# Performance work log

Measured on AMD Instinct MI355X. Metric: run time of the kernel, lower is better.

The kernel has to match this reference:

```python
import jax, jax.numpy as jnp
import numpy as np

B, T, D, HEADS = 2, 2048, 1024, 16


def setup_inputs() -> dict:
    key = jax.random.key(0)
    k1, k2, k3 = jax.random.split(key, 3)
    X = jax.random.normal(k1, (B, T, D), dtype=jnp.float32)
    W_KQV = jax.random.normal(k2, (D, 3 * D), dtype=jnp.float32) * 0.02
    W_out = jax.random.normal(k3, (D, D), dtype=jnp.float32) * 0.02
    # causal additive mask: -1e9 above the diagonal, 0 elsewhere
    mask = jnp.triu(jnp.full((T, T), -1e9, dtype=jnp.float32), k=1)
    return {"X": X, "W_KQV": W_KQV, "W_out": W_out, "mask": mask, "heads": HEADS}


def reference(X, W_KQV, W_out, mask, heads):
    b, t, d = X.shape
    hd = d // heads
    res = jnp.einsum('btd,de->bte', X, W_KQV)  # [B,T,3d]
    # needle module stacks split columns in K, Q, V order
    K, Q, V = jnp.split(res, 3, axis=-1)

    def to_heads(A):  # [B,T,d] -> [B,H,T,hd]
        return A.reshape(b, t, heads, hd).transpose(0, 2, 1, 3)

    K, Q, V = to_heads(K), to_heads(Q), to_heads(V)
    # NOTE: original computes K @ Q^T (not Q @ K^T) -- reproduced faithfully
    scores = jnp.einsum('bhkd,bhqd->bhkq', K, Q) / (hd ** 0.5) + mask  # [B,H,T,T]
    attn = jax.nn.softmax(scores, axis=-1)
    ctx = jnp.einsum('bhtq,bhqd->bhtd', attn, V)  # [B,H,T,hd]
    ctx = ctx.transpose(0, 2, 1, 3).reshape(b, t, d)
    out = jnp.einsum('btd,de->bte', ctx, W_out)  # [B,T,d]
    return out, attn
```

## Files before the change

### kernel.cpp

```cpp
#include <hip/hip_runtime.h>
#include <cstddef>

constexpr int B_ = 2, T_ = 2048, D_ = 1024, H_ = 16;

typedef __attribute__((ext_vector_type(8))) short short8;
typedef __attribute__((ext_vector_type(4))) float floatx4;

__device__ inline unsigned short f2bf(float f) {
    union { float f; unsigned int u; } v; v.f = f;
    unsigned int r = v.u + 0x7fffu + ((v.u >> 16) & 1u);
    return (unsigned short)(r >> 16);
}

#define GLD_LDS16(gptr, ldsptr)                                                        \
    __builtin_amdgcn_global_load_lds(                                                  \
        (const __attribute__((address_space(1))) void*)(gptr),                         \
        (__attribute__((address_space(3))) void*)(ldsptr), 16, 0, 0)

__global__ __launch_bounds__(256) void cast_bf16(const float* __restrict__ in,
                                                 unsigned short* __restrict__ out) {
    int idx = (blockIdx.x * 256 + threadIdx.x) * 8;
    float4 a = *(const float4*)(in + idx);
    float4 b = *(const float4*)(in + idx + 4);
    unsigned short tmp[8] = {f2bf(a.x), f2bf(a.y), f2bf(a.z), f2bf(a.w),
                             f2bf(b.x), f2bf(b.y), f2bf(b.z), f2bf(b.w)};
    *(uint4*)(out + idx) = *(const uint4*)tmp;
}

__global__ __launch_bounds__(256) void transpose_cast(const float* __restrict__ W,
                                                      unsigned short* __restrict__ Wt,
                                                      int K, int N) {
    const int k0 = blockIdx.y * 64, n0 = blockIdx.x * 64;
    __shared__ float t[64][65];
    const int tid = threadIdx.x;
    const int row = tid >> 4, c4 = (tid & 15) * 4;
#pragma unroll
    for (int r = 0; r < 4; r++) {
        float4 v = *(const float4*)&W[(size_t)(k0 + row + r * 16) * N + n0 + c4];
        t[row + r * 16][c4 + 0] = v.x; t[row + r * 16][c4 + 1] = v.y;
        t[row + r * 16][c4 + 2] = v.z; t[row + r * 16][c4 + 3] = v.w;
    }
    __syncthreads();
    const int n = tid >> 2, ks = (tid & 3) * 16;
    unsigned short o[16];
#pragma unroll
    for (int i = 0; i < 16; i++) o[i] = f2bf(t[ks + i][n]);
    unsigned short* dst = Wt + (size_t)(n0 + n) * K + k0 + ks;
    *(uint4*)dst = ((const uint4*)o)[0];
    *(uint4*)(dst + 8) = ((const uint4*)o)[1];
}

template <typename CT>
__global__ __launch_bounds__(256) void gemm_bt(const unsigned short* __restrict__ A,
                                               const unsigned short* __restrict__ Bt,
                                               CT* __restrict__ C, int M, int N, int K) {
    __shared__ unsigned short As[128 * 32];
    __shared__ unsigned short Bs[128 * 32];
    const int tid = threadIdx.x;
    const int lane = tid & 63, wave = tid >> 6;
    const int quad = lane >> 4, l16 = lane & 15;
    const int wr = wave >> 1, wc = wave & 1;
    const size_t bm = (size_t)blockIdx.y * 128, bn = (size_t)blockIdx.x * 128;
    const int r0 = tid >> 2, kc0 = (tid & 3) * 8;
    const unsigned short* Ap = A + bm * K;
    const unsigned short* Bp = Bt + bn * K;
    floatx4 acc[4][4] = {};
    for (int k0 = 0; k0 < K; k0 += 32) {
        GLD_LDS16(Ap + (size_t)r0 * K + k0 + kc0, &As[tid * 8]);
        GLD_LDS16(Ap + (size_t)(r0 + 64) * K + k0 + kc0, &As[(tid + 256) * 8]);
        GLD_LDS16(Bp + (size_t)r0 * K + k0 + kc0, &Bs[tid * 8]);
        GLD_LDS16(Bp + (size_t)(r0 + 64) * K + k0 + kc0, &Bs[(tid + 256) * 8]);
        __syncthreads();
        short8 af[4], bf[4];
#pragma unroll
        for (int i = 0; i < 4; i++)
            af[i] = *(const short8*)&As[(wr * 64 + i * 16 + l16) * 32 + quad * 8];
#pragma unroll
        for (int j = 0; j < 4; j++)
            bf[j] = *(const short8*)&Bs[(wc * 64 + j * 16 + l16) * 32 + quad * 8];
#pragma unroll
        for (int i = 0; i < 4; i++)
#pragma unroll
            for (int j = 0; j < 4; j++)
                acc[i][j] = __builtin_amdgcn_mfma_f32_16x16x32_bf16(af[i], bf[j], acc[i][j], 0, 0, 0);
        __syncthreads();
    }
#pragma unroll
    for (int i = 0; i < 4; i++) {
        size_t row0 = bm + wr * 64 + i * 16 + quad * 4;
#pragma unroll
        for (int j = 0; j < 4; j++) {
            size_t col = bn + wc * 64 + j * 16 + l16;
#pragma unroll
            for (int r = 0; r < 4; r++) {
                if constexpr (sizeof(CT) == 2)
                    C[(row0 + r) * N + col] = (CT)f2bf(acc[i][j][r]);
                else
                    C[(row0 + r) * N + col] = acc[i][j][r];
            }
        }
    }
}

__global__ __launch_bounds__(256) void scores_mfma(const unsigned short* __restrict__ resb,
                                                   float* __restrict__ attn) {
    const int bh = blockIdx.z, b = bh >> 4, h = bh & 15;
    const int bk = blockIdx.y * 128, bq = blockIdx.x * 128;
    float* S = attn + (size_t)bh * T_ * T_;
    const int tid = threadIdx.x;
    if (bq > bk) {
        const float4 z = make_float4(0.f, 0.f, 0.f, 0.f);
#pragma unroll
        for (int i = 0; i < 16; i++) {
            int idx = tid + i * 256;
            int row = idx >> 5, c4 = (idx & 31) * 4;
            *(float4*)&S[(size_t)(bk + row) * T_ + bq + c4] = z;
        }
        return;
    }
    __shared__ unsigned short Ks[128 * 64];
    __shared__ unsigned short Qs[128 * 64];
    const unsigned short* Kg = resb + (size_t)b * T_ * (3 * D_) + h * 64;
    const unsigned short* Qg = Kg + D_;
    const int row = tid >> 3, dc = (tid & 7) * 8;
#pragma unroll
    for (int r = 0; r < 4; r++) {
        GLD_LDS16(Kg + (size_t)(bk + row + r * 32) * (3 * D_) + dc, &Ks[(tid + r * 256) * 8]);
        GLD_LDS16(Qg + (size_t)(bq + row + r * 32) * (3 * D_) + dc, &Qs[(tid + r * 256) * 8]);
    }
    __syncthreads();
    const int lane = tid & 63, wave = tid >> 6;
    const int quad = lane >> 4, l16 = lane & 15;
    const int wr = wave >> 1, wc = wave & 1;
    floatx4 acc[4][4] = {};
#pragma unroll
    for (int ks = 0; ks < 2; ks++) {
        short8 af[4], bf[4];
#pragma unroll
        for (int i = 0; i < 4; i++)
            af[i] = *(const short8*)&Ks[(wr * 64 + i * 16 + l16) * 64 + ks * 32 + quad * 8];
#pragma unroll
        for (int j = 0; j < 4; j++)
            bf[j] = *(const short8*)&Qs[(wc * 64 + j * 16 + l16) * 64 + ks * 32 + quad * 8];
#pragma unroll
        for (int i = 0; i < 4; i++)
#pragma unroll
            for (int j = 0; j < 4; j++)
                acc[i][j] = __builtin_amdgcn_mfma_f32_16x16x32_bf16(af[i], bf[j], acc[i][j], 0, 0, 0);
    }
#pragma unroll
    for (int i = 0; i < 4; i++) {
        int k0r = bk + wr * 64 + i * 16 + quad * 4;
#pragma unroll
        for (int j = 0; j < 4; j++) {
            int q = bq + wc * 64 + j * 16 + l16;
#pragma unroll
            for (int r = 0; r < 4; r++) {
                int k = k0r + r;
                S[(size_t)k * T_ + q] = (q > k) ? -1e9f : acc[i][j][r] * 0.125f;
            }
        }
    }
}

__global__ __launch_bounds__(256) void softmax_causal(float* __restrict__ attn) {
    const size_t row = blockIdx.x;
    const int k = (int)(row & (T_ - 1));
    const int L = ((k >> 7) + 1) << 7;
    float* p = attn + row * (size_t)T_;
    const int t = threadIdx.x;
    float v[8];
    float m = -3.0e38f;
#pragma unroll
    for (int i = 0; i < 8; i++) {
        int q = t + i * 256;
        v[i] = (q < L) ? p[q] : -1e9f;
        m = fmaxf(m, v[i]);
    }
#pragma unroll
    for (int off = 32; off > 0; off >>= 1) m = fmaxf(m, __shfl_down(m, off, 64));
    __shared__ float redm[4], reds[4];
    const int wave = t >> 6, lane = t & 63;
    if (lane == 0) redm[wave] = m;
    __syncthreads();
    m = fmaxf(fmaxf(redm[0], redm[1]), fmaxf(redm[2], redm[3]));
    float s = 0.f;
#pragma unroll
    for (int i = 0; i < 8; i++) {
        v[i] = __expf(v[i] - m);
        s += v[i];
    }
#pragma unroll
    for (int off = 32; off > 0; off >>= 1) s += __shfl_down(s, off, 64);
    if (lane == 0) reds[wave] = s;
    __syncthreads();
    s = reds[0] + reds[1] + reds[2] + reds[3];
    const float inv = 1.0f / s;
#pragma unroll
    for (int i = 0; i < 8; i++) {
        int q = t + i * 256;
        if (q < L) p[q] = v[i] * inv;
    }
}

__global__ __launch_bounds__(256) void transpose_v(const unsigned short* __restrict__ resb,
                                                   unsigned short* __restrict__ Vt) {
    const int bh = blockIdx.y, b = bh >> 4, h = bh & 15;
    const int q0 = blockIdx.x * 64;
    __shared__ unsigned short t[64][66];
    const int tid = threadIdx.x;
    const unsigned short* Vg = resb + (size_t)b * T_ * (3 * D_) + 2 * D_ + h * 64;
    const int q = tid >> 3, c8 = (tid & 7) * 8;
#pragma unroll
    for (int r = 0; r < 2; r++) {
        int qq = q + r * 32;
        short8 v = *(const short8*)(Vg + (size_t)(q0 + qq) * (3 * D_) + c8);
#pragma unroll
        for (int i = 0; i < 8; i++) t[qq][c8 + i] = (unsigned short)v[i];
    }
    __syncthreads();
    const int c = tid >> 2, qs = (tid & 3) * 16;
    unsigned short o[16];
#pragma unroll
    for (int i = 0; i < 16; i++) o[i] = t[qs + i][c];
    unsigned short* dst = Vt + ((size_t)bh * 64 + c) * T_ + q0 + qs;
    *(uint4*)dst = ((const uint4*)o)[0];
    *(uint4*)(dst + 8) = ((const uint4*)o)[1];
}

__global__ __launch_bounds__(256) void ctx_mfma(const float* __restrict__ attn,
                                                const unsigned short* __restrict__ Vt,
                                                unsigned short* __restrict__ ctxb) {
    const int bh = blockIdx.y, b = bh >> 4, h = bh & 15;
    const int bt = blockIdx.x * 128;
    const float* Ag = attn + (size_t)bh * T_ * T_;
    const unsigned short* Bg = Vt + (size_t)bh * 64 * T_;
    __shared__ unsigned short As[128 * 40];
    __shared__ unsigned short Bs[64 * 32];
    const int tid = threadIdx.x;
    const int lane = tid & 63, wave = tid >> 6;
    const int quad = lane >> 4, l16 = lane & 15;
    const int wr = wave >> 1, wc = wave & 1;
    const int arow = tid >> 1, aq = (tid & 1) * 16;
    const int brow = tid >> 2, bq8 = (tid & 3) * 8;
    floatx4 acc[4][2] = {};
    const int qend = bt + 128;
    for (int q0 = 0; q0 < qend; q0 += 32) {
        const float* src = Ag + (size_t)(bt + arow) * T_ + q0 + aq;
        float4 v0 = *(const float4*)src;
        float4 v1 = *(const float4*)(src + 4);
        float4 v2 = *(const float4*)(src + 8);
        float4 v3 = *(const float4*)(src + 12);
        unsigned short tmp[16] = {f2bf(v0.x), f2bf(v0.y), f2bf(v0.z), f2bf(v0.w),
                                  f2bf(v1.x), f2bf(v1.y), f2bf(v1.z), f2bf(v1.w),
                                  f2bf(v2.x), f2bf(v2.y), f2bf(v2.z), f2bf(v2.w),
                                  f2bf(v3.x), f2bf(v3.y), f2bf(v3.z), f2bf(v3.w)};
        *(uint4*)&As[arow * 40 + aq] = ((const uint4*)tmp)[0];
        *(uint4*)&As[arow * 40 + aq + 8] = ((const uint4*)tmp)[1];
        GLD_LDS16(Bg + (size_t)brow * T_ + q0 + bq8, &Bs[tid * 8]);
        __syncthreads();
        short8 af[4], bf[2];
#pragma unroll
        for (int i = 0; i < 4; i++)
            af[i] = *(const short8*)&As[(wr * 64 + i * 16 + l16) * 40 + quad * 8];
#pragma unroll
        for (int j = 0; j < 2; j++)
            bf[j] = *(const short8*)&Bs[(wc * 32 + j * 16 + l16) * 32 + quad * 8];
#pragma unroll
        for (int i = 0; i < 4; i++)
#pragma unroll
            for (int j = 0; j < 2; j++)
                acc[i][j] = __builtin_amdgcn_mfma_f32_16x16x32_bf16(af[i], bf[j], acc[i][j], 0, 0, 0);
        __syncthreads();
    }
#pragma unroll
    for (int i = 0; i < 4; i++) {
        size_t t0 = (size_t)bt + wr * 64 + i * 16 + quad * 4;
#pragma unroll
        for (int j = 0; j < 2; j++) {
            int c = wc * 32 + j * 16 + l16;
#pragma unroll
            for (int r = 0; r < 4; r++)
                ctxb[((size_t)b * T_ + t0 + r) * D_ + h * 64 + c] = f2bf(acc[i][j][r]);
        }
    }
}

extern "C" void kernel_launch(void* const* d_in, const int* in_sizes, int n_in,
                              void* d_out, int out_size, void* d_ws, size_t ws_size,
                              hipStream_t stream) {
    const float* X = (const float*)d_in[0];
    const float* W_KQV = (const float*)d_in[1];
    const float* W_out = (const float*)d_in[2];
    float* out = (float*)d_out;
    float* attn = (float*)d_out + (size_t)B_ * T_ * D_;

    char* ws = (char*)d_ws;
    unsigned short* Xb = (unsigned short*)ws;
    unsigned short* Wt = (unsigned short*)(ws + (8u << 20));
    unsigned short* Wot = (unsigned short*)(ws + (14u << 20));
    unsigned short* resb = (unsigned short*)(ws + (16u << 20));
    unsigned short* Vt = (unsigned short*)(ws + (40u << 20));
    unsigned short* ctxb = (unsigned short*)(ws + (48u << 20));

    cast_bf16<<<(B_ * T_ * D_) / (8 * 256), 256, 0, stream>>>(X, Xb);
    transpose_cast<<<dim3((3 * D_) / 64, D_ / 64), 256, 0, stream>>>(W_KQV, Wt, D_, 3 * D_);
    transpose_cast<<<dim3(D_ / 64, D_ / 64), 256, 0, stream>>>(W_out, Wot, D_, D_);

    gemm_bt<unsigned short><<<dim3((3 * D_) / 128, (B_ * T_) / 128), 256, 0, stream>>>(
        Xb, Wt, resb, B_ * T_, 3 * D_, D_);

    transpose_v<<<dim3(T_ / 64, B_ * H_), 256, 0, stream>>>(resb, Vt);
    scores_mfma<<<dim3(T_ / 128, T_ / 128, B_ * H_), 256, 0, stream>>>(resb, attn);
    softmax_causal<<<B_ * H_ * T_, 256, 0, stream>>>(attn);
    ctx_mfma<<<dim3(T_ / 128, B_ * H_), 256, 0, stream>>>(attn, Vt, ctxb);

    gemm_bt<float><<<dim3(D_ / 128, (B_ * T_) / 128), 256, 0, stream>>>(
        ctxb, Wot, out, B_ * T_, D_, D_);
}
```

Baseline: 874.8 us.

## Fuse scores, softmax and context into one two-pass attention kernel; swizzle GEMM LDS

Replaces the separate scores, softmax and context kernels with one fused kernel per 128-row key tile. A first pass computes running row max and sum, and a second pass recomputes the scores, writes the normalized probabilities and accumulates P·V from LDS. This removes the extra read-modify-write passes over the large fp32 attention matrix, and the re-read of it in fp32. The GEMM now uses 64-wide K steps with an XOR-swizzled LDS layout and a two-blocks-per-CU launch bound. The cost is recomputing QK^T twice, and only 512 blocks with uneven per-block work because of the causal mask.

```diff
diff --git a/kernel.cpp b/kernel.cpp
--- a/kernel.cpp
+++ b/kernel.cpp
@@ -51,38 +51,48 @@
 }
 
 template <typename CT>
-__global__ __launch_bounds__(256) void gemm_bt(const unsigned short* __restrict__ A,
-                                               const unsigned short* __restrict__ Bt,
-                                               CT* __restrict__ C, int M, int N, int K) {
-    __shared__ unsigned short As[128 * 32];
-    __shared__ unsigned short Bs[128 * 32];
+__global__ __launch_bounds__(256, 2) void gemm_bt(const unsigned short* __restrict__ A,
+                                                  const unsigned short* __restrict__ Bt,
+                                                  CT* __restrict__ C, int M, int N, int K) {
+    __shared__ unsigned short As[128 * 64];
+    __shared__ unsigned short Bs[128 * 64];
     const int tid = threadIdx.x;
     const int lane = tid & 63, wave = tid >> 6;
     const int quad = lane >> 4, l16 = lane & 15;
     const int wr = wave >> 1, wc = wave & 1;
     const size_t bm = (size_t)blockIdx.y * 128, bn = (size_t)blockIdx.x * 128;
-    const int r0 = tid >> 2, kc0 = (tid & 3) * 8;
     const unsigned short* Ap = A + bm * K;
     const unsigned short* Bp = Bt + bn * K;
+    const int srow = tid >> 3, sc = tid & 7;
     floatx4 acc[4][4] = {};
-    for (int k0 = 0; k0 < K; k0 += 32) {
-        GLD_LDS16(Ap + (size_t)r0 * K + k0 + kc0, &As[tid * 8]);
-        GLD_LDS16(Ap + (size_t)(r0 + 64) * K + k0 + kc0, &As[(tid + 256) * 8]);
-        GLD_LDS16(Bp + (size_t)r0 * K + k0 + kc0, &Bs[tid * 8]);
-        GLD_LDS16(Bp + (size_t)(r0 + 64) * K + k0 + kc0, &Bs[(tid + 256) * 8]);
-        __syncthreads();
-        short8 af[4], bf[4];
-#pragma unroll
-        for (int i = 0; i < 4; i++)
-            af[i] = *(const short8*)&As[(wr * 64 + i * 16 + l16) * 32 + quad * 8];
-#pragma unroll
-        for (int j = 0; j < 4; j++)
-            bf[j] = *(const short8*)&Bs[(wc * 64 + j * 16 + l16) * 32 + quad * 8];
-#pragma unroll
-        for (int i = 0; i < 4; i++)
-#pragma unroll
-            for (int j = 0; j < 4; j++)
-                acc[i][j] = __builtin_amdgcn_mfma_f32_16x16x32_bf16(af[i], bf[j], acc[i][j], 0, 0, 0);
+    for (int k0 = 0; k0 < K; k0 += 64) {
+#pragma unroll
+        for (int it = 0; it < 4; it++) {
+            int rr = srow + it * 32;
+            int soff = k0 + ((sc ^ (rr & 7)) << 3);
+            GLD_LDS16(Ap + (size_t)rr * K + soff, &As[(tid + it * 256) * 8]);
+            GLD_LDS16(Bp + (size_t)rr * K + soff, &Bs[(tid + it * 256) * 8]);
+        }
+        __syncthreads();
+#pragma unroll
+        for (int ks = 0; ks < 2; ks++) {
+            short8 af[4], bf[4];
+#pragma unroll
+            for (int i = 0; i < 4; i++) {
+                int row = wr * 64 + i * 16 + l16, cf = ks * 4 + quad;
+                af[i] = *(const short8*)&As[row * 64 + ((cf ^ (row & 7)) << 3)];
+            }
+#pragma unroll
+            for (int j = 0; j < 4; j++) {
+                int row = wc * 64 + j * 16 + l16, cf = ks * 4 + quad;
+                bf[j] = *(const short8*)&Bs[row * 64 + ((cf ^ (row & 7)) << 3)];
+            }
+#pragma unroll
+            for (int i = 0; i < 4; i++)
+#pragma unroll
+                for (int j = 0; j < 4; j++)
+                    acc[i][j] = __builtin_amdgcn_mfma_f32_16x16x32_bf16(af[i], bf[j], acc[i][j], 0, 0, 0);
+        }
         __syncthreads();
     }
 #pragma unroll
@@ -99,107 +109,6 @@
                     C[(row0 + r) * N + col] = acc[i][j][r];
             }
         }
-    }
-}
-
-__global__ __launch_bounds__(256) void scores_mfma(const unsigned short* __restrict__ resb,
-                                                   float* __restrict__ attn) {
-    const int bh = blockIdx.z, b = bh >> 4, h = bh & 15;
-    const int bk = blockIdx.y * 128, bq = blockIdx.x * 128;
-    float* S = attn + (size_t)bh * T_ * T_;
-    const int tid = threadIdx.x;
-    if (bq > bk) {
-        const float4 z = make_float4(0.f, 0.f, 0.f, 0.f);
-#pragma unroll
-        for (int i = 0; i < 16; i++) {
-            int idx = tid + i * 256;
-            int row = idx >> 5, c4 = (idx & 31) * 4;
-            *(float4*)&S[(size_t)(bk + row) * T_ + bq + c4] = z;
-        }
-        return;
-    }
-    __shared__ unsigned short Ks[128 * 64];
-    __shared__ unsigned short Qs[128 * 64];
-    const unsigned short* Kg = resb + (size_t)b * T_ * (3 * D_) + h * 64;
-    const unsigned short* Qg = Kg + D_;
-    const int row = tid >> 3, dc = (tid & 7) * 8;
-#pragma unroll
-    for (int r = 0; r < 4; r++) {
-        GLD_LDS16(Kg + (size_t)(bk + row + r * 32) * (3 * D_) + dc, &Ks[(tid + r * 256) * 8]);
-        GLD_LDS16(Qg + (size_t)(bq + row + r * 32) * (3 * D_) + dc, &Qs[(tid + r * 256) * 8]);
-    }
-    __syncthreads();
-    const int lane = tid & 63, wave = tid >> 6;
-    const int quad = lane >> 4, l16 = lane & 15;
-    const int wr = wave >> 1, wc = wave & 1;
-    floatx4 acc[4][4] = {};
-#pragma unroll
-    for (int ks = 0; ks < 2; ks++) {
-        short8 af[4], bf[4];
-#pragma unroll
-        for (int i = 0; i < 4; i++)
-            af[i] = *(const short8*)&Ks[(wr * 64 + i * 16 + l16) * 64 + ks * 32 + quad * 8];
-#pragma unroll
-        for (int j = 0; j < 4; j++)
-            bf[j] = *(const short8*)&Qs[(wc * 64 + j * 16 + l16) * 64 + ks * 32 + quad * 8];
-#pragma unroll
-        for (int i = 0; i < 4; i++)
-#pragma unroll
-            for (int j = 0; j < 4; j++)
-                acc[i][j] = __builtin_amdgcn_mfma_f32_16x16x32_bf16(af[i], bf[j], acc[i][j], 0, 0, 0);
-    }
-#pragma unroll
-    for (int i = 0; i < 4; i++) {
-        int k0r = bk + wr * 64 + i * 16 + quad * 4;
-#pragma unroll
-        for (int j = 0; j < 4; j++) {
-            int q = bq + wc * 64 + j * 16 + l16;
-#pragma unroll
-            for (int r = 0; r < 4; r++) {
-                int k = k0r + r;
-                S[(size_t)k * T_ + q] = (q > k) ? -1e9f : acc[i][j][r] * 0.125f;
-            }
-        }
-    }
-}
-
-__global__ __launch_bounds__(256) void softmax_causal(float* __restrict__ attn) {
-    const size_t row = blockIdx.x;
-    const int k = (int)(row & (T_ - 1));
-    const int L = ((k >> 7) + 1) << 7;
-    float* p = attn + row * (size_t)T_;
-    const int t = threadIdx.x;
-    float v[8];
-    float m = -3.0e38f;
-#pragma unroll
-    for (int i = 0; i < 8; i++) {
-        int q = t + i * 256;
-        v[i] = (q < L) ? p[q] : -1e9f;
-        m = fmaxf(m, v[i]);
-    }
-#pragma unroll
-    for (int off = 32; off > 0; off >>= 1) m = fmaxf(m, __shfl_down(m, off, 64));
-    __shared__ float redm[4], reds[4];
-    const int wave = t >> 6, lane = t & 63;
-    if (lane == 0) redm[wave] = m;
-    __syncthreads();
-    m = fmaxf(fmaxf(redm[0], redm[1]), fmaxf(redm[2], redm[3]));
-    float s = 0.f;
-#pragma unroll
-    for (int i = 0; i < 8; i++) {
-        v[i] = __expf(v[i] - m);
-        s += v[i];
-    }
-#pragma unroll
-    for (int off = 32; off > 0; off >>= 1) s += __shfl_down(s, off, 64);
-    if (lane == 0) reds[wave] = s;
-    __syncthreads();
-    s = reds[0] + reds[1] + reds[2] + reds[3];
-    const float inv = 1.0f / s;
-#pragma unroll
-    for (int i = 0; i < 8; i++) {
-        int q = t + i * 256;
-        if (q < L) p[q] = v[i] * inv;
     }
 }
 
@@ -228,60 +137,215 @@
     *(uint4*)(dst + 8) = ((const uint4*)o)[1];
 }
 
-__global__ __launch_bounds__(256) void ctx_mfma(const float* __restrict__ attn,
-                                                const unsigned short* __restrict__ Vt,
-                                                unsigned short* __restrict__ ctxb) {
+__global__ __launch_bounds__(256, 2) void attn_fused(const unsigned short* __restrict__ resb,
+                                                     const unsigned short* __restrict__ Vt,
+                                                     float* __restrict__ attn,
+                                                     unsigned short* __restrict__ ctxb) {
     const int bh = blockIdx.y, b = bh >> 4, h = bh & 15;
-    const int bt = blockIdx.x * 128;
-    const float* Ag = attn + (size_t)bh * T_ * T_;
-    const unsigned short* Bg = Vt + (size_t)bh * 64 * T_;
-    __shared__ unsigned short As[128 * 40];
-    __shared__ unsigned short Bs[64 * 32];
+    const int kt = 15 - (int)blockIdx.x;
+    const int k0 = kt * 128;
+    float* S = attn + (size_t)bh * T_ * T_;
+
+    __shared__ char smem[53760];
+    unsigned short* KV = (unsigned short*)smem;
+    unsigned short* QP = (unsigned short*)(smem + 16896);
+    float* mpart = (float*)(smem + 16896 + 33792);
+    float* lpart = mpart + 256;
+    float* mfin = lpart + 256;
+    float* linv = mfin + 128;
+
     const int tid = threadIdx.x;
     const int lane = tid & 63, wave = tid >> 6;
     const int quad = lane >> 4, l16 = lane & 15;
     const int wr = wave >> 1, wc = wave & 1;
-    const int arow = tid >> 1, aq = (tid & 1) * 16;
-    const int brow = tid >> 2, bq8 = (tid & 3) * 8;
-    floatx4 acc[4][2] = {};
-    const int qend = bt + 128;
-    for (int q0 = 0; q0 < qend; q0 += 32) {
-        const float* src = Ag + (size_t)(bt + arow) * T_ + q0 + aq;
-        float4 v0 = *(const float4*)src;
-        float4 v1 = *(const float4*)(src + 4);
-        float4 v2 = *(const float4*)(src + 8);
-        float4 v3 = *(const float4*)(src + 12);
-        unsigned short tmp[16] = {f2bf(v0.x), f2bf(v0.y), f2bf(v0.z), f2bf(v0.w),
-                                  f2bf(v1.x), f2bf(v1.y), f2bf(v1.z), f2bf(v1.w),
-                                  f2bf(v2.x), f2bf(v2.y), f2bf(v2.z), f2bf(v2.w),
-                                  f2bf(v3.x), f2bf(v3.y), f2bf(v3.z), f2bf(v3.w)};
-        *(uint4*)&As[arow * 40 + aq] = ((const uint4*)tmp)[0];
-        *(uint4*)&As[arow * 40 + aq + 8] = ((const uint4*)tmp)[1];
-        GLD_LDS16(Bg + (size_t)brow * T_ + q0 + bq8, &Bs[tid * 8]);
-        __syncthreads();
-        short8 af[4], bf[2];
+
+    const unsigned short* Kg = resb + (size_t)b * T_ * (3 * D_) + h * 64;
+    const unsigned short* Qg = Kg + D_;
+    const unsigned short* Vg = Vt + (size_t)bh * 64 * T_;
+
+    {
+        const int qz0 = (kt + 1) * 128, ZW = T_ - qz0;
+        const float4 z = make_float4(0.f, 0.f, 0.f, 0.f);
+        for (int row = wave; row < 128; row += 4)
+            for (int c = lane * 4; c < ZW; c += 256)
+                *(float4*)&S[(size_t)(k0 + row) * T_ + qz0 + c] = z;
+    }
+
+    const int srow = tid >> 3, sc = tid & 7;
+#pragma unroll
+    for (int it = 0; it < 4; it++) {
+        int rr = srow + it * 32;
+        GLD_LDS16(Kg + (size_t)(k0 + rr) * (3 * D_) + ((sc ^ (rr & 7)) << 3),
+                  &KV[(tid + it * 256) * 8]);
+    }
+    __syncthreads();
+    short8 af_k[4][2];
+#pragma unroll
+    for (int i = 0; i < 4; i++)
+#pragma unroll
+        for (int ks = 0; ks < 2; ks++) {
+            int row = wr * 64 + i * 16 + l16, cf = ks * 4 + quad;
+            af_k[i][ks] = *(const short8*)&KV[row * 64 + ((cf ^ (row & 7)) << 3)];
+        }
+    __syncthreads();
+
+    float m_run[4][4], l_run[4][4];
+#pragma unroll
+    for (int i = 0; i < 4; i++)
+#pragma unroll
+        for (int r = 0; r < 4; r++) { m_run[i][r] = -3.0e38f; l_run[i][r] = 0.f; }
+
+    for (int qt = 0; qt <= kt; qt++) {
+        const int q0 = qt * 128;
+#pragma unroll
+        for (int it = 0; it < 4; it++) {
+            int rr = srow + it * 32;
+            GLD_LDS16(Qg + (size_t)(q0 + rr) * (3 * D_) + ((sc ^ (rr & 7)) << 3),
+                      &QP[(tid + it * 256) * 8]);
+        }
+        __syncthreads();
+        short8 bf[4][2];
+#pragma unroll
+        for (int j = 0; j < 4; j++)
+#pragma unroll
+            for (int ks = 0; ks < 2; ks++) {
+                int row = wc * 64 + j * 16 + l16, cf = ks * 4 + quad;
+                bf[j][ks] = *(const short8*)&QP[row * 64 + ((cf ^ (row & 7)) << 3)];
+            }
+        __syncthreads();
+        floatx4 acc[4][4] = {};
+#pragma unroll
+        for (int ks = 0; ks < 2; ks++)
+#pragma unroll
+            for (int i = 0; i < 4; i++)
+#pragma unroll
+                for (int j = 0; j < 4; j++)
+                    acc[i][j] = __builtin_amdgcn_mfma_f32_16x16x32_bf16(af_k[i][ks], bf[j][ks], acc[i][j], 0, 0, 0);
+        const bool dm = (qt == kt);
 #pragma unroll
         for (int i = 0; i < 4; i++)
-            af[i] = *(const short8*)&As[(wr * 64 + i * 16 + l16) * 40 + quad * 8];
-#pragma unroll
-        for (int j = 0; j < 2; j++)
-            bf[j] = *(const short8*)&Bs[(wc * 32 + j * 16 + l16) * 32 + quad * 8];
+#pragma unroll
+            for (int r = 0; r < 4; r++) {
+                const int krow = wr * 64 + i * 16 + quad * 4 + r;
+                float vv[4];
+#pragma unroll
+                for (int j = 0; j < 4; j++) {
+                    int ql = wc * 64 + j * 16 + l16;
+                    float s = acc[i][j][r] * 0.125f;
+                    vv[j] = (dm && ql > krow) ? -3.0e38f : s;
+                }
+                float mt = fmaxf(fmaxf(vv[0], vv[1]), fmaxf(vv[2], vv[3]));
+#pragma unroll
+                for (int msk = 1; msk < 16; msk <<= 1)
+                    mt = fmaxf(mt, __shfl_xor(mt, msk, 64));
+                float mn = fmaxf(m_run[i][r], mt);
+                float corr = __expf(m_run[i][r] - mn);
+                float lt = __expf(vv[0] - mn) + __expf(vv[1] - mn) +
+                           __expf(vv[2] - mn) + __expf(vv[3] - mn);
+                l_run[i][r] = l_run[i][r] * corr + lt;
+                m_run[i][r] = mn;
+            }
+    }
+#pragma unroll
+    for (int i = 0; i < 4; i++)
+#pragma unroll
+        for (int r = 0; r < 4; r++) {
+            float lv = l_run[i][r];
+#pragma unroll
+            for (int msk = 1; msk < 16; msk <<= 1) lv += __shfl_xor(lv, msk, 64);
+            if (l16 == 0) {
+                int row = wr * 64 + i * 16 + quad * 4 + r;
+                mpart[wc * 128 + row] = m_run[i][r];
+                lpart[wc * 128 + row] = lv;
+            }
+        }
+    __syncthreads();
+    if (tid < 128) {
+        float m0 = mpart[tid], m1 = mpart[128 + tid];
+        float m = fmaxf(m0, m1);
+        float l = lpart[tid] * __expf(m0 - m) + lpart[128 + tid] * __expf(m1 - m);
+        mfin[tid] = m;
+        linv[tid] = 1.0f / l;
+    }
+    __syncthreads();
+
+    floatx4 cacc[4][2] = {};
+    for (int qt = 0; qt <= kt; qt++) {
+        const int q0 = qt * 128;
+#pragma unroll
+        for (int it = 0; it < 4; it++) {
+            int rr = srow + it * 32;
+            GLD_LDS16(Qg + (size_t)(q0 + rr) * (3 * D_) + ((sc ^ (rr & 7)) << 3),
+                      &QP[(tid + it * 256) * 8]);
+        }
+#pragma unroll
+        for (int it = 0; it < 4; it++) {
+            int ci = tid + it * 256;
+            int row = ci >> 4, ch = ci & 15;
+            short8 v = *(const short8*)&Vg[(size_t)row * T_ + q0 + ch * 8];
+            *(short8*)&KV[row * 132 + ch * 8] = v;
+        }
+        __syncthreads();
+        short8 bf[4][2];
+#pragma unroll
+        for (int j = 0; j < 4; j++)
+#pragma unroll
+            for (int ks = 0; ks < 2; ks++) {
+                int row = wc * 64 + j * 16 + l16, cf = ks * 4 + quad;
+                bf[j][ks] = *(const short8*)&QP[row * 64 + ((cf ^ (row & 7)) << 3)];
+            }
+        floatx4 acc[4][4] = {};
+#pragma unroll
+        for (int ks = 0; ks < 2; ks++)
+#pragma unroll
+            for (int i = 0; i < 4; i++)
+#pragma unroll
+                for (int j = 0; j < 4; j++)
+                    acc[i][j] = __builtin_amdgcn_mfma_f32_16x16x32_bf16(af_k[i][ks], bf[j][ks], acc[i][j], 0, 0, 0);
+        __syncthreads();
+        const bool dm = (qt == kt);
 #pragma unroll
         for (int i = 0; i < 4; i++)
 #pragma unroll
-            for (int j = 0; j < 2; j++)
-                acc[i][j] = __builtin_amdgcn_mfma_f32_16x16x32_bf16(af[i], bf[j], acc[i][j], 0, 0, 0);
+            for (int r = 0; r < 4; r++) {
+                const int krow = wr * 64 + i * 16 + quad * 4 + r;
+                const float mv = mfin[krow], li = linv[krow];
+#pragma unroll
+                for (int j = 0; j < 4; j++) {
+                    int ql = wc * 64 + j * 16 + l16;
+                    float p = __expf(acc[i][j][r] * 0.125f - mv) * li;
+                    if (dm && ql > krow) p = 0.f;
+                    S[(size_t)(k0 + krow) * T_ + q0 + ql] = p;
+                    QP[krow * 132 + ql] = f2bf(p);
+                }
+            }
+        __syncthreads();
+#pragma unroll
+        for (int ks2 = 0; ks2 < 4; ks2++) {
+            short8 ap[4], bv[2];
+#pragma unroll
+            for (int i = 0; i < 4; i++)
+                ap[i] = *(const short8*)&QP[(wr * 64 + i * 16 + l16) * 132 + ks2 * 32 + quad * 8];
+#pragma unroll
+            for (int j2 = 0; j2 < 2; j2++)
+                bv[j2] = *(const short8*)&KV[(wc * 32 + j2 * 16 + l16) * 132 + ks2 * 32 + quad * 8];
+#pragma unroll
+            for (int i = 0; i < 4; i++)
+#pragma unroll
+                for (int j2 = 0; j2 < 2; j2++)
+                    cacc[i][j2] = __builtin_amdgcn_mfma_f32_16x16x32_bf16(ap[i], bv[j2], cacc[i][j2], 0, 0, 0);
+        }
         __syncthreads();
     }
 #pragma unroll
     for (int i = 0; i < 4; i++) {
-        size_t t0 = (size_t)bt + wr * 64 + i * 16 + quad * 4;
-#pragma unroll
-        for (int j = 0; j < 2; j++) {
-            int c = wc * 32 + j * 16 + l16;
+        size_t t0 = (size_t)k0 + wr * 64 + i * 16 + quad * 4;
+#pragma unroll
+        for (int j2 = 0; j2 < 2; j2++) {
+            int c = wc * 32 + j2 * 16 + l16;
 #pragma unroll
             for (int r = 0; r < 4; r++)
-                ctxb[((size_t)b * T_ + t0 + r) * D_ + h * 64 + c] = f2bf(acc[i][j][r]);
+                ctxb[((size_t)b * T_ + t0 + r) * D_ + h * 64 + c] = f2bf(cacc[i][j2][r]);
         }
     }
 }
@@ -311,9 +375,8 @@
         Xb, Wt, resb, B_ * T_, 3 * D_, D_);
 
     transpose_v<<<dim3(T_ / 64, B_ * H_), 256, 0, stream>>>(resb, Vt);
-    scores_mfma<<<dim3(T_ / 128, T_ / 128, B_ * H_), 256, 0, stream>>>(resb, attn);
-    softmax_causal<<<B_ * H_ * T_, 256, 0, stream>>>(attn);
-    ctx_mfma<<<dim3(T_ / 128, B_ * H_), 256, 0, stream>>>(attn, Vt, ctxb);
+
+    attn_fused<<<dim3(16, B_ * H_), 256, 0, stream>>>(resb, Vt, attn, ctxb);
 
     gemm_bt<float><<<dim3(D_ / 128, (B_ * T_) / 128), 256, 0, stream>>>(
         ctxb, Wot, out, B_ * T_, D_, D_);
```

Result: faster. 805.6 us (-7.9%).
